# Optimization experiments

Hardware: AMD Instinct MI355X
Metric: run time of the kernel (lower is better)

The kernel has to match this reference:

```python
import jax, jax.numpy as jnp
import numpy as np

DIM = 2048
N_HEADS = 16
HEAD_DIM = DIM // N_HEADS
GROUP_SIZE = 128
THRESHOLD = 0.5
EPS = 1e-8
B, T = 2, 2048


def _ternary_dequant(w):
    # groupwise absmean ternary quantize + dequant; DIM % GROUP_SIZE == 0 so no pad
    O, I = w.shape
    g = I // GROUP_SIZE
    wg = w.reshape(O, g, GROUP_SIZE)
    scale = jnp.clip(jnp.mean(jnp.abs(wg), axis=-1, keepdims=True), EPS)
    wn = wg / scale
    q = jnp.where(wn > THRESHOLD, 1.0, jnp.where(wn < -THRESHOLD, -1.0, 0.0))
    return (q * scale).reshape(O, I)


def _bitlinear(x, w):
    # STE: forward uses quantized weight
    w_ste = w + jax.lax.stop_gradient(_ternary_dequant(w) - w)
    return x @ w_ste.T


def _rope_tables(t, head_dim, base=10000.0):
    half = head_dim // 2
    inv_freq = 1.0 / (base ** (jnp.arange(half, dtype=jnp.float32) / half))
    freqs = jnp.outer(jnp.arange(t, dtype=jnp.float32), inv_freq)  # [T, half]
    return jnp.cos(freqs), jnp.sin(freqs)


def _apply_rope(x, cos, sin):
    # x: [B, H, T, D]
    d = x.shape[-1]
    x1, x2 = x[..., : d // 2], x[..., d // 2 :]
    cos = cos[None, None, :, :]
    sin = sin[None, None, :, :]
    return jnp.concatenate([x1 * cos - x2 * sin, x1 * sin + x2 * cos], axis=-1)


def setup_inputs() -> dict:
    key = jax.random.key(0)
    ks = jax.random.split(key, 5)
    std = 1.0 / np.sqrt(DIM)
    return {
        "x": jax.random.normal(ks[0], (B, T, DIM), dtype=jnp.float32),
        "w_q": jax.random.normal(ks[1], (DIM, DIM), dtype=jnp.float32) * std,
        "w_k": jax.random.normal(ks[2], (DIM, DIM), dtype=jnp.float32) * std,
        "w_v": jax.random.normal(ks[3], (DIM, DIM), dtype=jnp.float32) * std,
        "w_o": jax.random.normal(ks[4], (DIM, DIM), dtype=jnp.float32) * std,
    }


def reference(x, w_q, w_k, w_v, w_o):
    b, t, c = x.shape
    scale = HEAD_DIM ** -0.5

    def split_heads(y):
        return y.reshape(b, t, N_HEADS, HEAD_DIM).transpose(0, 2, 1, 3)  # [B,H,T,D]

    q = split_heads(_bitlinear(x, w_q))
    k = split_heads(_bitlinear(x, w_k))
    v = split_heads(_bitlinear(x, w_v))

    cos, sin = _rope_tables(t, HEAD_DIM)
    q = _apply_rope(q, cos, sin)
    k = _apply_rope(k, cos, sin)

    scores = jnp.einsum("bhqd,bhkd->bhqk", q, k) * scale
    causal = jnp.triu(jnp.ones((t, t), dtype=bool), k=1)
    scores = jnp.where(causal[None, None], -jnp.inf, scores)
    probs = jax.nn.softmax(scores, axis=-1)
    y = jnp.einsum("bhqk,bhkd->bhqd", probs, v)
    y = y.transpose(0, 2, 1, 3).reshape(b, t, c)
    return _bitlinear(y, w_o)
```

## Files before the change

kernel.cpp:

```cpp
#include <hip/hip_runtime.h>
#include <stdint.h>
#include <math.h>

#define DIMC 2048
#define NHEADS 16
#define HDIM 128
#define TSEQ 2048
#define NTOK 4096

using bf16x8 = __attribute__((ext_vector_type(8))) short;
using f32x4  = __attribute__((ext_vector_type(4))) float;

typedef __attribute__((address_space(1))) const void gas_void;
typedef __attribute__((address_space(3))) void las_void;

static __device__ __forceinline__ unsigned short f2b(float f) {
  union { float f; unsigned int u; } a; a.f = f;
  unsigned int u = a.u;
  u = (u + 0x7fffu + ((u >> 16) & 1u)) >> 16;
  return (unsigned short)u;
}
static __device__ __forceinline__ float b2f(unsigned short s) {
  union { unsigned int u; float f; } a; a.u = ((unsigned int)s) << 16;
  return a.f;
}

static __device__ __forceinline__ int detect_inline(const void* __restrict__ x)
{
  const int lane = threadIdx.x & 63;
  const unsigned short u = ((const unsigned short*)x)[2 * lane];
  const int e = (u >> 7) & 0xFF;
  const unsigned long long m = __ballot((e >= 112) && (e <= 135));
  return (__popcll(m) >= 32) ? 1 : 0;
}

static __device__ __forceinline__ void dequant_one(
    const void* __restrict__ w, unsigned short* __restrict__ o,
    int grp, int lane, int isbf16)
{
  float a, bq;
  if (isbf16) {
    const unsigned int pk =
        ((const unsigned int*)((const unsigned short*)w + (long)grp * 128))[lane];
    a  = b2f((unsigned short)(pk & 0xffffu));
    bq = b2f((unsigned short)(pk >> 16));
  } else {
    const float2 v = ((const float2*)((const float*)w + (long)grp * 128))[lane];
    a = v.x; bq = v.y;
  }
  double s = fabs((double)a) + fabs((double)bq);
  #pragma unroll
  for (int off = 1; off < 64; off <<= 1) s += __shfl_xor(s, off);
  double scale = s * (1.0 / 128.0);
  if (scale < 1e-8) scale = 1e-8;
  const float fs = (float)scale;
  const double hs = 0.5 * scale;
  const double da = (double)a, db = (double)bq;
  const float q0 = (da > hs) ? fs : ((da < -hs) ? -fs : 0.0f);
  const float q1 = (db > hs) ? fs : ((db < -hs) ? -fs : 0.0f);
  const unsigned int opk = (unsigned int)f2b(q0) | ((unsigned int)f2b(q1) << 16);
  ((unsigned int*)o)[(long)grp * 64 + lane] = opk;
}

__global__ void __launch_bounds__(256) prep(
    const void* __restrict__ x,
    const void* __restrict__ w0, const void* __restrict__ w1,
    const void* __restrict__ w2, const void* __restrict__ w3,
    unsigned short* __restrict__ xb, unsigned short* __restrict__ wqkv,
    unsigned short* __restrict__ wob)
{
  const int isbf16 = detect_inline(x);
  const int wave = threadIdx.x >> 6, lane = threadIdx.x & 63;
  const int y = blockIdx.y;
  if (y == 0) {
    const int i = (blockIdx.x * 256 + threadIdx.x) * 4;
    if (isbf16) {
      *(ushort4*)(xb + i) = *(const ushort4*)((const unsigned short*)x + i);
    } else {
      const float4 v = *(const float4*)((const float*)x + i);
      ushort4 u;
      u.x = f2b(v.x); u.y = f2b(v.y); u.z = f2b(v.z); u.w = f2b(v.w);
      *(ushort4*)(xb + i) = u;
    }
  } else if (y <= 3) {
    const void* w = (y == 1) ? w0 : (y == 2) ? w1 : w2;
    dequant_one(w, wqkv + (long)(y - 1) * DIMC * DIMC,
                blockIdx.x * 4 + wave, lane, isbf16);
  } else {
    dequant_one(w3, wob, blockIdx.x * 4 + wave, lane, isbf16);
  }
}

__global__ void __launch_bounds__(256) dequant_auto(
    const void* __restrict__ w, const void* __restrict__ x,
    unsigned short* __restrict__ o)
{
  const int isbf16 = detect_inline(x);
  dequant_one(w, o, blockIdx.x * 4 + (threadIdx.x >> 6), threadIdx.x & 63,
              isbf16);
}

static __device__ __forceinline__ void gemm8_core(
    const unsigned short* __restrict__ A, const unsigned short* __restrict__ Bm,
    int m0, int n0, int K, f32x4 (&acc)[4][4],
    unsigned short (*smA)[2][8192], unsigned short (*smB)[8192])
{
  const int tid = threadIdx.x;
  const int w = tid >> 6, lane = tid & 63;
  const int wr = w >> 1, wc = w & 1;
  const int c16 = lane & 15, q4 = lane >> 4;
  const int swz = (c16 * 32 + q4 * 8) ^ ((c16 & 8) ? 16 : 0);
  const int srow = lane >> 2;
  const int scol = ((lane & 3) * 8) ^ ((lane & 32) ? 16 : 0);
  const int rg0 = w >> 1, cg = w & 1;
  const int NT = K >> 6;

  #pragma unroll
  for (int i = 0; i < 4; i++)
    #pragma unroll
    for (int j = 0; j < 4; j++) acc[i][j] = (f32x4){0.f, 0.f, 0.f, 0.f};

  auto stage = [&](const unsigned short* __restrict__ G, int rowbase, int kt,
                   unsigned short* dst) {
    #pragma unroll
    for (int l = 0; l < 2; l++) {
      const unsigned short* s = G +
          (long)(rowbase + (rg0 + l * 4) * 16 + srow) * K + kt * 64 + cg * 32 + scol;
      __builtin_amdgcn_global_load_lds((gas_void*)s,
          (las_void*)(dst + (l * 8 + w) * 512), 16, 0, 0);
    }
  };

  stage(A,  m0,       0, smA[0][0]);
  stage(A,  m0 + 128, 0, smA[0][1]);
  stage(Bm, n0,       0, smB[0]);
  stage(A,  m0,       1, smA[1][0]);
  stage(A,  m0 + 128, 1, smA[1][1]);
  stage(Bm, n0,       1, smB[1]);
  asm volatile("s_waitcnt vmcnt(6)" ::: "memory");
  __builtin_amdgcn_s_barrier();

  bf16x8 af[4][2], b01[2][2], b23[2][2];
  const int ah = wr >> 1;
  const int abase = (wr & 1) * 4096;
  const int bbase = wc * 4096;

  int ai = 0, a2 = 2;
  for (int t = 0; t < NT; ++t) {
    const int bi = t & 1;

    #pragma unroll
    for (int m = 0; m < 4; m++)
      #pragma unroll
      for (int kk = 0; kk < 2; kk++)
        af[m][kk] = *(const bf16x8*)&smA[ai][ah][abase + m * 1024 + kk * 512 + swz];
    #pragma unroll
    for (int n = 0; n < 2; n++)
      #pragma unroll
      for (int kk = 0; kk < 2; kk++) {
        b01[n][kk] = *(const bf16x8*)&smB[bi][bbase + n * 1024 + kk * 512 + swz];
        b23[n][kk] = *(const bf16x8*)&smB[bi][bbase + (2 + n) * 1024 + kk * 512 + swz];
      }
    if (t + 2 < NT) {
      stage(A, m0,       t + 2, smA[a2][0]);
      stage(A, m0 + 128, t + 2, smA[a2][1]);
    }
    __builtin_amdgcn_s_barrier();
    asm volatile("s_waitcnt lgkmcnt(0)" ::: "memory");
    __builtin_amdgcn_s_setprio(1);
    #pragma unroll
    for (int kk = 0; kk < 2; kk++)
      #pragma unroll
      for (int m = 0; m < 4; m++)
        #pragma unroll
        for (int n = 0; n < 2; n++)
          acc[m][n] = __builtin_amdgcn_mfma_f32_16x16x32_bf16(
              af[m][kk], b01[n][kk], acc[m][n], 0, 0, 0);
    __builtin_amdgcn_s_setprio(0);
    __builtin_amdgcn_s_barrier();

    if (t + 2 < NT) stage(Bm, n0, t + 2, smB[bi]);
    __builtin_amdgcn_s_setprio(1);
    #pragma unroll
    for (int kk = 0; kk < 2; kk++)
      #pragma unroll
      for (int m = 0; m < 4; m++)
        #pragma unroll
        for (int n = 0; n < 2; n++)
          acc[m][2 + n] = __builtin_amdgcn_mfma_f32_16x16x32_bf16(
              af[m][kk], b23[n][kk], acc[m][2 + n], 0, 0, 0);
    __builtin_amdgcn_s_setprio(0);
    if (t + 1 < NT) {
      if (t + 2 < NT) { asm volatile("s_waitcnt vmcnt(6)" ::: "memory"); }
      else            { asm volatile("s_waitcnt vmcnt(0)" ::: "memory"); }
      __builtin_amdgcn_s_barrier();
    }
    ai = (ai == 2) ? 0 : ai + 1;
    a2 = (a2 == 2) ? 0 : a2 + 1;
  }
}

__global__ void __launch_bounds__(512, 2) gemm8_qkv(
    const unsigned short* __restrict__ A, const unsigned short* __restrict__ Bm,
    unsigned short* __restrict__ C0, unsigned short* __restrict__ C1,
    unsigned short* __restrict__ C2, int K)
{
  __shared__ unsigned short smA[3][2][8192];
  __shared__ unsigned short smB[2][8192];
  const int n0 = blockIdx.x * 128;
  const int m0 = blockIdx.y * 256;
  f32x4 acc[4][4];
  gemm8_core(A, Bm, m0, n0, K, acc, smA, smB);

  unsigned short* Cb = (n0 < 2048) ? C0 : (n0 < 4096) ? C1 : C2;
  const int w = threadIdx.x >> 6, lane = threadIdx.x & 63;
  const int wr = w >> 1, wc = w & 1;
  const int c16 = lane & 15, q4 = lane >> 4;
  const int nloc = (n0 & 2047) + wc * 64;
  #pragma unroll
  for (int mt = 0; mt < 4; mt++) {
    const int m = m0 + wr * 64 + mt * 16 + q4 * 4;
    #pragma unroll
    for (int nt = 0; nt < 4; nt++) {
      const int n = nloc + nt * 16 + c16;
      #pragma unroll
      for (int r = 0; r < 4; r++)
        Cb[(long)(m + r) * DIMC + n] = f2b(acc[mt][nt][r]);
    }
  }
}

__global__ void __launch_bounds__(512, 2) gemm8_bt(
    const unsigned short* __restrict__ A, const unsigned short* __restrict__ Bm,
    float* __restrict__ C, int N, int K)
{
  __shared__ unsigned short smA[3][2][8192];
  __shared__ unsigned short smB[2][8192];
  const int n0 = blockIdx.x * 128;
  const int m0 = blockIdx.y * 256;
  f32x4 acc[4][4];
  gemm8_core(A, Bm, m0, n0, K, acc, smA, smB);

  const int w = threadIdx.x >> 6, lane = threadIdx.x & 63;
  const int wr = w >> 1, wc = w & 1;
  const int c16 = lane & 15, q4 = lane >> 4;
  #pragma unroll
  for (int mt = 0; mt < 4; mt++) {
    const int m = m0 + wr * 64 + mt * 16 + q4 * 4;
    #pragma unroll
    for (int nt = 0; nt < 4; nt++) {
      const int n = n0 + wc * 64 + nt * 16 + c16;
      #pragma unroll
      for (int r = 0; r < 4; r++)
        C[(long)(m + r) * N + n] = acc[mt][nt][r];
    }
  }
}

__global__ void __launch_bounds__(256) rope_kernel(
    unsigned short* __restrict__ Q, unsigned short* __restrict__ Kb)
{
  const int idx = blockIdx.x * 256 + threadIdx.x;
  const int d4 = (idx & 15) * 4;
  const int h = (idx >> 4) & (NHEADS - 1);
  const int row = idx >> 8;
  const int t = row & (TSEQ - 1);
  const long base = (long)row * DIMC + h * HDIM + d4;

  ushort4 q1 = *(ushort4*)(Q + base), q2 = *(ushort4*)(Q + base + 64);
  ushort4 k1 = *(ushort4*)(Kb + base), k2 = *(ushort4*)(Kb + base + 64);
  unsigned short* q1p = (unsigned short*)&q1;
  unsigned short* q2p = (unsigned short*)&q2;
  unsigned short* k1p = (unsigned short*)&k1;
  unsigned short* k2p = (unsigned short*)&k2;

  #pragma unroll
  for (int j = 0; j < 4; j++) {
    const int d = d4 + j;
    const float inv_freq = expf(-9.210340371976184f * (float)d * (1.0f / 64.0f));
    float sn, cs;
    sincosf((float)t * inv_freq, &sn, &cs);
    float x1 = b2f(q1p[j]), x2 = b2f(q2p[j]);
    q1p[j] = f2b(x1 * cs - x2 * sn);
    q2p[j] = f2b(x1 * sn + x2 * cs);
    x1 = b2f(k1p[j]); x2 = b2f(k2p[j]);
    k1p[j] = f2b(x1 * cs - x2 * sn);
    k2p[j] = f2b(x1 * sn + x2 * cs);
  }
  *(ushort4*)(Q + base) = q1;  *(ushort4*)(Q + base + 64) = q2;
  *(ushort4*)(Kb + base) = k1; *(ushort4*)(Kb + base + 64) = k2;
}

#define FA_M 16.0f
__global__ void __launch_bounds__(256) fattn(
    const unsigned short* __restrict__ Q,
    const unsigned short* __restrict__ K,
    const unsigned short* __restrict__ V,
    unsigned short* __restrict__ Y)
{
  __shared__ unsigned short SU[9216];
  __shared__ unsigned short VT[128 * 72];
  __shared__ float red[4][32];

  const int tid = threadIdx.x, wave = tid >> 6, lane = tid & 63;
  const int idx = blockIdx.x;
  const int qt = 15 - (idx >> 5);
  const int bh = idx & 31;
  const int b = bh >> 4, h = bh & 15;
  const int qbase = qt * 128;
  const int qw = wave * 32;
  const int c = lane & 15, g = lane >> 4;
  const long tokbase = (long)b * TSEQ;
  const int col0 = h * HDIM;

  bf16x8 qf[2][4];
  #pragma unroll
  for (int qq = 0; qq < 2; qq++) {
    const unsigned short* qp =
        Q + (tokbase + qbase + qw + qq * 16 + c) * DIMC + col0 + g * 8;
    #pragma unroll
    for (int kc = 0; kc < 4; kc++) qf[qq][kc] = *(const bf16x8*)(qp + kc * 32);
  }

  f32x4 od[8][2];
  #pragma unroll
  for (int dt = 0; dt < 8; dt++)
    #pragma unroll
    for (int qq = 0; qq < 2; qq++)
      od[dt][qq] = (f32x4){0.f, 0.f, 0.f, 0.f};
  float lpart[2][4];
  #pragma unroll
  for (int qq = 0; qq < 2; qq++)
    #pragma unroll
    for (int r = 0; r < 4; r++) lpart[qq][r] = 0.0f;

  const int ksr = tid >> 2, ksc = (tid & 3) * 32;
  const int vk0 = (tid & 31) * 2, vd0 = (tid >> 5) * 16;

  const float SC = 0.088388347648318447f;
  const int nkt = 2 * qt + 2;

  float4 kr0, kr1, kr2, kr3;
  bf16x8 va0, va1, vb0, vb1;
  {
    const unsigned short* src = K + (tokbase + ksr) * DIMC + col0 + ksc;
    kr0 = ((const float4*)src)[0]; kr1 = ((const float4*)src)[1];
    kr2 = ((const float4*)src)[2]; kr3 = ((const float4*)src)[3];
    const unsigned short* s0 = V + (tokbase + vk0) * DIMC + col0 + vd0;
    const unsigned short* s1 = s0 + DIMC;
    va0 = *(const bf16x8*)(s0); va1 = *(const bf16x8*)(s0 + 8);
    vb0 = *(const bf16x8*)(s1); vb1 = *(const bf16x8*)(s1 + 8);
  }

  for (int kt = 0; kt < nkt; kt++) {
    const int kb = kt * 64;
    __syncthreads();
    {
      float4* dst = (float4*)&SU[ksr * 136 + ksc];
      dst[0] = kr0; dst[1] = kr1; dst[2] = kr2; dst[3] = kr3;
    }
    {
      #pragma unroll
      for (int dd = 0; dd < 8; dd++) {
        const unsigned int p0 =
            (unsigned int)(unsigned short)va0[dd] |
            ((unsigned int)(unsigned short)vb0[dd] << 16);
        *(unsigned int*)&VT[(vd0 + dd) * 72 + vk0] = p0;
      }
      #pragma unroll
      for (int dd = 0; dd < 8; dd++) {
        const unsigned int p1 =
            (unsigned int)(unsigned short)va1[dd] |
            ((unsigned int)(unsigned short)vb1[dd] << 16);
        *(unsigned int*)&VT[(vd0 + 8 + dd) * 72 + vk0] = p1;
      }
    }
    __syncthreads();

    if (kt + 1 < nkt) {
      const int kb2 = kb + 64;
      const unsigned short* src = K + (tokbase + kb2 + ksr) * DIMC + col0 + ksc;
      kr0 = ((const float4*)src)[0]; kr1 = ((const float4*)src)[1];
      kr2 = ((const float4*)src)[2]; kr3 = ((const float4*)src)[3];
      const unsigned short* s0 = V + (tokbase + kb2 + vk0) * DIMC + col0 + vd0;
      const unsigned short* s1 = s0 + DIMC;
      va0 = *(const bf16x8*)(s0); va1 = *(const bf16x8*)(s0 + 8);
      vb0 = *(const bf16x8*)(s1); vb1 = *(const bf16x8*)(s1 + 8);
    }

    f32x4 sacc[2][4];
    #pragma unroll
    for (int qq = 0; qq < 2; qq++)
      #pragma unroll
      for (int nt = 0; nt < 4; nt++) sacc[qq][nt] = (f32x4){0.f, 0.f, 0.f, 0.f};
    #pragma unroll
    for (int kc = 0; kc < 4; kc++) {
      bf16x8 bk[4];
      #pragma unroll
      for (int nt = 0; nt < 4; nt++)
        bk[nt] = *(const bf16x8*)&SU[(nt * 16 + c) * 136 + kc * 32 + g * 8];
      #pragma unroll
      for (int qq = 0; qq < 2; qq++)
        #pragma unroll
        for (int nt = 0; nt < 4; nt++)
          sacc[qq][nt] = __builtin_amdgcn_mfma_f32_16x16x32_bf16(
              qf[qq][kc], bk[nt], sacc[qq][nt], 0, 0, 0);
    }
    __syncthreads();

    #pragma unroll
    for (int qq = 0; qq < 2; qq++)
      #pragma unroll
      for (int r = 0; r < 4; r++) {
        const int qg = qbase + qw + qq * 16 + g * 4 + r;
        #pragma unroll
        for (int nt = 0; nt < 4; nt++) {
          const int kg = kb + nt * 16 + c;
          const float sv = sacc[qq][nt][r] * SC - FA_M;
          const float p = (kg > qg) ? 0.0f : __expf(sv);
          lpart[qq][r] += p;
          SU[(wave * 32 + qq * 16 + g * 4 + r) * 72 + nt * 16 + c] = f2b(p);
        }
      }

    #pragma unroll
    for (int kc = 0; kc < 2; kc++) {
      bf16x8 pb[2];
      #pragma unroll
      for (int qq = 0; qq < 2; qq++)
        pb[qq] = *(const bf16x8*)&SU[(wave * 32 + qq * 16 + c) * 72 + kc * 32 + g * 8];
      #pragma unroll
      for (int dt = 0; dt < 8; dt++) {
        bf16x8 va = *(const bf16x8*)&VT[(dt * 16 + c) * 72 + kc * 32 + g * 8];
        #pragma unroll
        for (int qq = 0; qq < 2; qq++)
          od[dt][qq] = __builtin_amdgcn_mfma_f32_16x16x32_bf16(
              va, pb[qq], od[dt][qq], 0, 0, 0);
      }
    }
  }

  #pragma unroll
  for (int qq = 0; qq < 2; qq++)
    #pragma unroll
    for (int r = 0; r < 4; r++) {
      float l = lpart[qq][r];
      #pragma unroll
      for (int off = 1; off < 16; off <<= 1) l += __shfl_xor(l, off);
      lpart[qq][r] = l;
    }
  __syncthreads();
  if (c == 0) {
    #pragma unroll
    for (int qq = 0; qq < 2; qq++)
      #pragma unroll
      for (int r = 0; r < 4; r++)
        red[wave][qq * 16 + g * 4 + r] = 1.0f / lpart[qq][r];
  }
  __syncthreads();
  #pragma unroll
  for (int qq = 0; qq < 2; qq++) {
    const float linv = red[wave][qq * 16 + c];
    unsigned short* yp =
        Y + (tokbase + qbase + qw + qq * 16 + c) * DIMC + col0;
    #pragma unroll
    for (int dt = 0; dt < 8; dt++)
      #pragma unroll
      for (int r = 0; r < 4; r++)
        yp[dt * 16 + g * 4 + r] = f2b(od[dt][qq][r] * linv);
  }
}

extern "C" void kernel_launch(void* const* d_in, const int* in_sizes, int n_in,
                              void* d_out, int out_size, void* d_ws, size_t ws_size,
                              hipStream_t stream)
{
  const void* x  = d_in[0];
  const void* wq = d_in[1];
  const void* wk = d_in[2];
  const void* wv = d_in[3];
  const void* wo = d_in[4];
  float* out = (float*)d_out;

  char* ws = (char*)d_ws;
  const size_t MB = 1024 * 1024;
  unsigned short* wbuf = (unsigned short*)(ws + 0 * MB);
  unsigned short* xb   = (unsigned short*)(ws + 24 * MB);
  unsigned short* Qb   = (unsigned short*)(ws + 40 * MB);
  unsigned short* Kb   = (unsigned short*)(ws + 56 * MB);
  unsigned short* Vb   = (unsigned short*)(ws + 72 * MB);
  unsigned short* wob  = (unsigned short*)(ws + 88 * MB);
  unsigned short* Yb   = xb;

  const int wo_in_prep = (ws_size >= 97 * MB) ? 1 : 0;

  prep<<<dim3(8192, wo_in_prep ? 5 : 4), 256, 0, stream>>>(
      x, wq, wk, wv, wo, xb, wbuf, wob);
  gemm8_qkv<<<dim3(48, 16), 512, 0, stream>>>(xb, wbuf, Qb, Kb, Vb, DIMC);
  rope_kernel<<<dim3(4096), 256, 0, stream>>>(Qb, Kb);
  fattn<<<dim3(512), 256, 0, stream>>>(Qb, Kb, Vb, Yb);
  const unsigned short* wo_b;
  if (wo_in_prep) {
    wo_b = wob;
  } else {
    dequant_auto<<<dim3(8192), 256, 0, stream>>>(wo, x, wbuf);
    wo_b = wbuf;
  }
  gemm8_bt<<<dim3(16, 16), 512, 0, stream>>>(Yb, wo_b, out, DIMC, DIMC);
}
```

Baseline: 393.3 us.

## Use 256x256-tile QKV GEMM with double-buffered LDS and batch prep work per block

Replaces the 256x128-tile QKV projection GEMM with a new 256x256-tile kernel. Each 512-thread block computes 8x4 MFMA tiles per wave, and global-to-LDS staging of A and B is interleaved between four MFMA phases with double buffering. This raises arithmetic intensity per loaded byte and halves B-tile reloads, at the cost of one block per CU (launch bound 1) and heavier register use. The prep kernel also processes four chunks per block, cutting its grid fourfold to lower block launch overhead.

```diff
diff --git a/kernel.cpp b/kernel.cpp
--- a/kernel.cpp
+++ b/kernel.cpp
@@ -73,21 +73,28 @@
   const int wave = threadIdx.x >> 6, lane = threadIdx.x & 63;
   const int y = blockIdx.y;
   if (y == 0) {
-    const int i = (blockIdx.x * 256 + threadIdx.x) * 4;
-    if (isbf16) {
-      *(ushort4*)(xb + i) = *(const ushort4*)((const unsigned short*)x + i);
-    } else {
-      const float4 v = *(const float4*)((const float*)x + i);
-      ushort4 u;
-      u.x = f2b(v.x); u.y = f2b(v.y); u.z = f2b(v.z); u.w = f2b(v.w);
-      *(ushort4*)(xb + i) = u;
+    #pragma unroll
+    for (int it = 0; it < 4; it++) {
+      const int i = ((blockIdx.x * 4 + it) * 256 + threadIdx.x) * 4;
+      if (isbf16) {
+        *(ushort4*)(xb + i) = *(const ushort4*)((const unsigned short*)x + i);
+      } else {
+        const float4 v = *(const float4*)((const float*)x + i);
+        ushort4 u;
+        u.x = f2b(v.x); u.y = f2b(v.y); u.z = f2b(v.z); u.w = f2b(v.w);
+        *(ushort4*)(xb + i) = u;
+      }
     }
   } else if (y <= 3) {
     const void* w = (y == 1) ? w0 : (y == 2) ? w1 : w2;
-    dequant_one(w, wqkv + (long)(y - 1) * DIMC * DIMC,
-                blockIdx.x * 4 + wave, lane, isbf16);
+    unsigned short* oo = wqkv + (long)(y - 1) * DIMC * DIMC;
+    #pragma unroll
+    for (int it = 0; it < 4; it++)
+      dequant_one(w, oo, (blockIdx.x * 4 + it) * 4 + wave, lane, isbf16);
   } else {
-    dequant_one(w3, wob, blockIdx.x * 4 + wave, lane, isbf16);
+    #pragma unroll
+    for (int it = 0; it < 4; it++)
+      dequant_one(w3, wob, (blockIdx.x * 4 + it) * 4 + wave, lane, isbf16);
   }
 }
 
@@ -200,10 +207,9 @@
   }
 }
 
-__global__ void __launch_bounds__(512, 2) gemm8_qkv(
+__global__ void __launch_bounds__(512, 2) gemm8_bt(
     const unsigned short* __restrict__ A, const unsigned short* __restrict__ Bm,
-    unsigned short* __restrict__ C0, unsigned short* __restrict__ C1,
-    unsigned short* __restrict__ C2, int K)
+    float* __restrict__ C, int N, int K)
 {
   __shared__ unsigned short smA[3][2][8192];
   __shared__ unsigned short smB[2][8192];
@@ -212,47 +218,167 @@
   f32x4 acc[4][4];
   gemm8_core(A, Bm, m0, n0, K, acc, smA, smB);
 
-  unsigned short* Cb = (n0 < 2048) ? C0 : (n0 < 4096) ? C1 : C2;
   const int w = threadIdx.x >> 6, lane = threadIdx.x & 63;
   const int wr = w >> 1, wc = w & 1;
   const int c16 = lane & 15, q4 = lane >> 4;
-  const int nloc = (n0 & 2047) + wc * 64;
   #pragma unroll
   for (int mt = 0; mt < 4; mt++) {
     const int m = m0 + wr * 64 + mt * 16 + q4 * 4;
     #pragma unroll
     for (int nt = 0; nt < 4; nt++) {
+      const int n = n0 + wc * 64 + nt * 16 + c16;
+      #pragma unroll
+      for (int r = 0; r < 4; r++)
+        C[(long)(m + r) * N + n] = acc[mt][nt][r];
+    }
+  }
+}
+
+__global__ void __launch_bounds__(512, 1) gemm256_qkv(
+    const unsigned short* __restrict__ A, const unsigned short* __restrict__ Bm,
+    unsigned short* __restrict__ C0, unsigned short* __restrict__ C1,
+    unsigned short* __restrict__ C2)
+{
+  __shared__ unsigned short sm[2][2][2][8192];
+  const int K = DIMC, NT = K >> 6;
+
+  const int tid = threadIdx.x;
+  const int w = tid >> 6, lane = tid & 63;
+  const int wr = w >> 2, wc = w & 3;
+  const int wh = wc >> 1, wb = (wc & 1) * 4;
+  const int c16 = lane & 15, q4 = lane >> 4;
+  const int swz = (c16 * 32 + q4 * 8) ^ ((c16 & 8) ? 16 : 0);
+  const int srow = lane >> 2;
+  const int scol = ((lane & 3) * 8) ^ ((lane & 32) ? 16 : 0);
+  const int rg0 = w >> 1, cg = w & 1;
+
+  const int m0 = blockIdx.x * 256;
+  const int n0 = blockIdx.y * 256;
+
+  f32x4 acc[8][4];
+  #pragma unroll
+  for (int i = 0; i < 8; i++)
+    #pragma unroll
+    for (int j = 0; j < 4; j++) acc[i][j] = (f32x4){0.f, 0.f, 0.f, 0.f};
+
+  auto stage = [&](const unsigned short* __restrict__ G, int rowbase, int kt,
+                   unsigned short* dst) {
+    #pragma unroll
+    for (int l = 0; l < 2; l++) {
+      const unsigned short* s = G +
+          (long)(rowbase + (rg0 + l * 4) * 16 + srow) * K + kt * 64 + cg * 32 + scol;
+      __builtin_amdgcn_global_load_lds((gas_void*)s,
+          (las_void*)(dst + (l * 8 + w) * 512), 16, 0, 0);
+    }
+  };
+
+  stage(A,  m0,       0, &sm[0][0][0][0]);
+  stage(A,  m0 + 128, 0, &sm[0][0][1][0]);
+  stage(Bm, n0,       0, &sm[0][1][0][0]);
+  stage(Bm, n0 + 128, 0, &sm[0][1][1][0]);
+  stage(Bm, n0,       1, &sm[1][1][0][0]);
+  stage(Bm, n0 + 128, 1, &sm[1][1][1][0]);
+  asm volatile("s_waitcnt vmcnt(4)" ::: "memory");
+  __builtin_amdgcn_s_barrier();
+
+  bf16x8 af[4][2], b01[2][2], b23[2][2];
+
+  for (int t = 0; t < NT; ++t) {
+    const int cur = t & 1, nxt = cur ^ 1;
+
+    #pragma unroll
+    for (int m = 0; m < 4; m++)
+      #pragma unroll
+      for (int kk = 0; kk < 2; kk++)
+        af[m][kk] = *(const bf16x8*)&sm[cur][0][wr][m * 1024 + kk * 512 + swz];
+    #pragma unroll
+    for (int n = 0; n < 2; n++)
+      #pragma unroll
+      for (int kk = 0; kk < 2; kk++)
+        b01[n][kk] = *(const bf16x8*)&sm[cur][1][wh][(wb + n) * 1024 + kk * 512 + swz];
+    if (t + 1 < NT) stage(A, m0, t + 1, &sm[nxt][0][0][0]);
+    __builtin_amdgcn_s_barrier();
+    asm volatile("s_waitcnt lgkmcnt(0)" ::: "memory");
+    __builtin_amdgcn_s_setprio(1);
+    #pragma unroll
+    for (int kk = 0; kk < 2; kk++)
+      #pragma unroll
+      for (int m = 0; m < 4; m++)
+        #pragma unroll
+        for (int n = 0; n < 2; n++)
+          acc[m][n] = __builtin_amdgcn_mfma_f32_16x16x32_bf16(
+              af[m][kk], b01[n][kk], acc[m][n], 0, 0, 0);
+    __builtin_amdgcn_s_setprio(0);
+    __builtin_amdgcn_s_barrier();
+
+    #pragma unroll
+    for (int n = 0; n < 2; n++)
+      #pragma unroll
+      for (int kk = 0; kk < 2; kk++)
+        b23[n][kk] = *(const bf16x8*)&sm[cur][1][wh][(wb + 2 + n) * 1024 + kk * 512 + swz];
+    if (t + 1 < NT) stage(A, m0 + 128, t + 1, &sm[nxt][0][1][0]);
+    __builtin_amdgcn_s_barrier();
+    asm volatile("s_waitcnt lgkmcnt(0)" ::: "memory");
+    __builtin_amdgcn_s_setprio(1);
+    #pragma unroll
+    for (int kk = 0; kk < 2; kk++)
+      #pragma unroll
+      for (int m = 0; m < 4; m++)
+        #pragma unroll
+        for (int n = 0; n < 2; n++)
+          acc[m][2 + n] = __builtin_amdgcn_mfma_f32_16x16x32_bf16(
+              af[m][kk], b23[n][kk], acc[m][2 + n], 0, 0, 0);
+    __builtin_amdgcn_s_setprio(0);
+    __builtin_amdgcn_s_barrier();
+
+    #pragma unroll
+    for (int m = 0; m < 4; m++)
+      #pragma unroll
+      for (int kk = 0; kk < 2; kk++)
+        af[m][kk] = *(const bf16x8*)&sm[cur][0][wr][(4 + m) * 1024 + kk * 512 + swz];
+    if (t + 2 < NT) stage(Bm, n0, t + 2, &sm[cur][1][0][0]);
+    __builtin_amdgcn_s_barrier();
+    asm volatile("s_waitcnt lgkmcnt(0)" ::: "memory");
+    __builtin_amdgcn_s_setprio(1);
+    #pragma unroll
+    for (int kk = 0; kk < 2; kk++)
+      #pragma unroll
+      for (int m = 0; m < 4; m++)
+        #pragma unroll
+        for (int n = 0; n < 2; n++)
+          acc[4 + m][2 + n] = __builtin_amdgcn_mfma_f32_16x16x32_bf16(
+              af[m][kk], b23[n][kk], acc[4 + m][2 + n], 0, 0, 0);
+    __builtin_amdgcn_s_setprio(0);
+    __builtin_amdgcn_s_barrier();
+
+    if (t + 2 < NT) stage(Bm, n0 + 128, t + 2, &sm[cur][1][1][0]);
+    __builtin_amdgcn_s_barrier();
+    __builtin_amdgcn_s_setprio(1);
+    #pragma unroll
+    for (int kk = 0; kk < 2; kk++)
+      #pragma unroll
+      for (int m = 0; m < 4; m++)
+        #pragma unroll
+        for (int n = 0; n < 2; n++)
+          acc[4 + m][n] = __builtin_amdgcn_mfma_f32_16x16x32_bf16(
+              af[m][kk], b01[n][kk], acc[4 + m][n], 0, 0, 0);
+    __builtin_amdgcn_s_setprio(0);
+    if (t + 2 < NT) { asm volatile("s_waitcnt vmcnt(4)" ::: "memory"); }
+    else            { asm volatile("s_waitcnt vmcnt(0)" ::: "memory"); }
+    __builtin_amdgcn_s_barrier();
+  }
+
+  unsigned short* Cb = (n0 < 2048) ? C0 : (n0 < 4096) ? C1 : C2;
+  const int nloc = (n0 & 2047) + wc * 64;
+  #pragma unroll
+  for (int mt = 0; mt < 8; mt++) {
+    const int m = m0 + wr * 128 + mt * 16 + q4 * 4;
+    #pragma unroll
+    for (int nt = 0; nt < 4; nt++) {
       const int n = nloc + nt * 16 + c16;
       #pragma unroll
       for (int r = 0; r < 4; r++)
         Cb[(long)(m + r) * DIMC + n] = f2b(acc[mt][nt][r]);
-    }
-  }
-}
-
-__global__ void __launch_bounds__(512, 2) gemm8_bt(
-    const unsigned short* __restrict__ A, const unsigned short* __restrict__ Bm,
-    float* __restrict__ C, int N, int K)
-{
-  __shared__ unsigned short smA[3][2][8192];
-  __shared__ unsigned short smB[2][8192];
-  const int n0 = blockIdx.x * 128;
-  const int m0 = blockIdx.y * 256;
-  f32x4 acc[4][4];
-  gemm8_core(A, Bm, m0, n0, K, acc, smA, smB);
-
-  const int w = threadIdx.x >> 6, lane = threadIdx.x & 63;
-  const int wr = w >> 1, wc = w & 1;
-  const int c16 = lane & 15, q4 = lane >> 4;
-  #pragma unroll
-  for (int mt = 0; mt < 4; mt++) {
-    const int m = m0 + wr * 64 + mt * 16 + q4 * 4;
-    #pragma unroll
-    for (int nt = 0; nt < 4; nt++) {
-      const int n = n0 + wc * 64 + nt * 16 + c16;
-      #pragma unroll
-      for (int r = 0; r < 4; r++)
-        C[(long)(m + r) * N + n] = acc[mt][nt][r];
     }
   }
 }
@@ -494,9 +620,9 @@
 
   const int wo_in_prep = (ws_size >= 97 * MB) ? 1 : 0;
 
-  prep<<<dim3(8192, wo_in_prep ? 5 : 4), 256, 0, stream>>>(
+  prep<<<dim3(2048, wo_in_prep ? 5 : 4), 256, 0, stream>>>(
       x, wq, wk, wv, wo, xb, wbuf, wob);
-  gemm8_qkv<<<dim3(48, 16), 512, 0, stream>>>(xb, wbuf, Qb, Kb, Vb, DIMC);
+  gemm256_qkv<<<dim3(16, 24), 512, 0, stream>>>(xb, wbuf, Qb, Kb, Vb);
   rope_kernel<<<dim3(4096), 256, 0, stream>>>(Qb, Kb);
   fattn<<<dim3(512), 256, 0, stream>>>(Qb, Kb, Vb, Yb);
   const unsigned short* wo_b;
```

After: 386.4 us. No clear change (-1.8%).
